# Optimization experiments

Measured on AMD Instinct MI355X. Metric: run time of the kernel, lower is better.

The kernel has to match this reference:

```python
import jax, jax.numpy as jnp
import numpy as np

ITERATIONS = 3
OUT_CAPS, OUT_DIM = 10, 16


def squash(x):
    # square_norm / (1 + square_norm) * x / (sqrt(square_norm) + 1e-6), norm over last axis
    sn = jnp.sum(x * x, axis=-1, keepdims=True)
    return sn / (1.0 + sn) * x / (jnp.sqrt(sn) + 1e-6)


def setup_inputs() -> dict:
    key = jax.random.key(0)
    kx, kw = jax.random.split(key)
    x = jax.random.normal(kx, (256, 32, 6, 6, 8), dtype=jnp.float32)
    W = 0.01 * jax.random.normal(kw, (1, 32, 6, 6, 10, 8, 16), dtype=jnp.float32)
    return {"x": x, "W": W}


def reference(x, W):
    w = W[0]  # [i,j,k,o,d,e]
    # u_hat: prediction vectors, [B, i, j, k, O, E]
    u_hat = jnp.einsum('bijkd,ijkode->bijkoe', x, w)
    u_det = jax.lax.stop_gradient(u_hat)
    b = jnp.zeros(u_hat.shape[:-1], dtype=u_hat.dtype)  # [B,i,j,k,O]
    for _ in range(ITERATIONS - 1):
        c = jax.nn.softmax(b, axis=-1)
        s = jnp.einsum('bijko,bijkoe->boe', c, u_det)   # reduce over all input-capsule axes
        v = squash(s)                                    # [B,O,E]
        b = b + jnp.einsum('bijkoe,boe->bijko', u_det, v)
    c = jax.nn.softmax(b, axis=-1)
    s = jnp.einsum('bijko,bijkoe->boe', c, u_hat)
    v = squash(s)
    return v.reshape(-1, OUT_CAPS, OUT_DIM)
```

## Files before the change

### kernel.cpp

```cpp
#include <hip/hip_runtime.h>
#include <math.h>

#define BATCH 256
#define IC    1152
#define DD    8
#define OO    10
#define EE    16
#define BTILE 128
#define NBT   2
#define NT    640
#define CHUNK 9
#define NCHUNK 128

__global__ __launch_bounds__(NT) void caps_pass_kernel(
    const float* __restrict__ x,
    const float* __restrict__ W,
    const float* __restrict__ V,
    float* __restrict__ s_part,
    int first)
{
    __shared__ float x_lds[2][DD][BTILE];
    __shared__ float logit_lds[2][2][OO][64];

    const int tid = threadIdx.x;
    const int o   = tid >> 6;
    const int bl  = tid & 63;
    const int o_u = __builtin_amdgcn_readfirstlane(o);
    const int b0  = blockIdx.y * BTILE + bl;
    const int b1  = b0 + 64;
    const int ijk0 = blockIdx.x * CHUNK;

    float v0[EE], v1[EE];
    if (first) {
        #pragma unroll
        for (int e = 0; e < EE; ++e) { v0[e] = 0.f; v1[e] = 0.f; }
    } else {
        const float4* vp0 = reinterpret_cast<const float4*>(V + ((size_t)b0 * OO + o) * EE);
        const float4* vp1 = reinterpret_cast<const float4*>(V + ((size_t)b1 * OO + o) * EE);
        #pragma unroll
        for (int q = 0; q < 4; ++q) {
            float4 t0 = vp0[q], t1 = vp1[q];
            v0[q*4+0]=t0.x; v0[q*4+1]=t0.y; v0[q*4+2]=t0.z; v0[q*4+3]=t0.w;
            v1[q*4+0]=t1.x; v1[q*4+1]=t1.y; v1[q*4+2]=t1.z; v1[q*4+3]=t1.w;
        }
    }

    float s0[EE], s1[EE];
    #pragma unroll
    for (int e = 0; e < EE; ++e) { s0[e] = 0.f; s1[e] = 0.f; }

    const bool loader = tid < BTILE * 2;
    const int lb = tid >> 1;
    const int lq = tid & 1;
    const float* xbase = x + (size_t)(blockIdx.y * BTILE + lb) * (IC * DD) + lq * 4;

    float4 xpre = make_float4(0.f, 0.f, 0.f, 0.f);
    if (loader) {
        xpre = *reinterpret_cast<const float4*>(xbase + (size_t)ijk0 * DD);
        x_lds[0][lq*4+0][lb] = xpre.x;
        x_lds[0][lq*4+1][lb] = xpre.y;
        x_lds[0][lq*4+2][lb] = xpre.z;
        x_lds[0][lq*4+3][lb] = xpre.w;
    }
    __syncthreads();

    int p = 0;
    for (int r = 0; r < CHUNK; ++r) {
        const int ijk = ijk0 + r;

        if (r + 1 < CHUNK && loader)
            xpre = *reinterpret_cast<const float4*>(xbase + (size_t)(ijk + 1) * DD);

        const float* wp = W + (size_t)ijk * (OO * DD * EE) + o_u * (DD * EE);
        float u0[EE], u1[EE];
        #pragma unroll
        for (int e = 0; e < EE; ++e) { u0[e] = 0.f; u1[e] = 0.f; }
        #pragma unroll
        for (int d = 0; d < DD; ++d) {
            float x0 = x_lds[p][d][bl];
            float x1 = x_lds[p][d][bl + 64];
            #pragma unroll
            for (int e = 0; e < EE; ++e) {
                float w = wp[d * EE + e];
                u0[e] = fmaf(x0, w, u0[e]);
                u1[e] = fmaf(x1, w, u1[e]);
            }
        }

        float lg0 = 0.f, lg1 = 0.f;
        if (!first) {
            #pragma unroll
            for (int e = 0; e < EE; ++e) {
                lg0 = fmaf(u0[e], v0[e], lg0);
                lg1 = fmaf(u1[e], v1[e], lg1);
            }
            logit_lds[p][0][o][bl] = lg0;
            logit_lds[p][1][o][bl] = lg1;
        }

        if (r + 1 < CHUNK && loader) {
            x_lds[p^1][lq*4+0][lb] = xpre.x;
            x_lds[p^1][lq*4+1][lb] = xpre.y;
            x_lds[p^1][lq*4+2][lb] = xpre.z;
            x_lds[p^1][lq*4+3][lb] = xpre.w;
        }

        __syncthreads();

        float c0, c1;
        if (first) {
            c0 = 0.1f; c1 = 0.1f;
        } else {
            float l0[OO], l1[OO];
            #pragma unroll
            for (int oo = 0; oo < OO; ++oo) {
                l0[oo] = logit_lds[p][0][oo][bl];
                l1[oo] = logit_lds[p][1][oo][bl];
            }
            float m0 = -1e30f, m1 = -1e30f;
            #pragma unroll
            for (int oo = 0; oo < OO; ++oo) {
                m0 = fmaxf(m0, l0[oo]);
                m1 = fmaxf(m1, l1[oo]);
            }
            float d0 = 0.f, d1 = 0.f;
            #pragma unroll
            for (int oo = 0; oo < OO; ++oo) {
                d0 += __expf(l0[oo] - m0);
                d1 += __expf(l1[oo] - m1);
            }
            c0 = __expf(lg0 - m0) / d0;
            c1 = __expf(lg1 - m1) / d1;
        }

        #pragma unroll
        for (int e = 0; e < EE; ++e) {
            s0[e] = fmaf(c0, u0[e], s0[e]);
            s1[e] = fmaf(c1, u1[e], s1[e]);
        }
        p ^= 1;
    }

    float* sp0 = s_part + (((size_t)blockIdx.x * BATCH + b0) * OO + o) * EE;
    float* sp1 = s_part + (((size_t)blockIdx.x * BATCH + b1) * OO + o) * EE;
    #pragma unroll
    for (int q = 0; q < 4; ++q) {
        float4 t0, t1;
        t0.x = s0[q*4+0]; t0.y = s0[q*4+1]; t0.z = s0[q*4+2]; t0.w = s0[q*4+3];
        t1.x = s1[q*4+0]; t1.y = s1[q*4+1]; t1.z = s1[q*4+2]; t1.w = s1[q*4+3];
        reinterpret_cast<float4*>(sp0)[q] = t0;
        reinterpret_cast<float4*>(sp1)[q] = t1;
    }
}

__global__ __launch_bounds__(256) void caps_squash_kernel(
    const float* __restrict__ s_part,
    float* __restrict__ V,
    float* __restrict__ out,
    int accum, int last)
{
    const int g = blockIdx.x * 256 + threadIdx.x;
    float s = 0.f;
    #pragma unroll 8
    for (int ch = 0; ch < NCHUNK; ++ch)
        s += s_part[(size_t)ch * (BATCH * OO * EE) + g];

    float sq = s * s;
    #pragma unroll
    for (int m = 1; m < 16; m <<= 1) sq += __shfl_xor(sq, m, 16);

    float scale = sq / (1.f + sq) / (sqrtf(sq) + 1e-6f);
    float v = scale * s;

    if (last)       out[g] = v;
    else if (accum) V[g]  += v;
    else            V[g]   = v;
}

extern "C" void kernel_launch(void* const* d_in, const int* in_sizes, int n_in,
                              void* d_out, int out_size, void* d_ws, size_t ws_size,
                              hipStream_t stream) {
    const float* x = (const float*)d_in[0];
    const float* W = (const float*)d_in[1];
    float* out = (float*)d_out;

    float* s_part = (float*)d_ws;
    float* V      = s_part + (size_t)NCHUNK * BATCH * OO * EE;

    dim3 grid(NCHUNK, NBT), blk(NT);
    const int sq_blocks = (BATCH * OO * EE) / 256;

    caps_pass_kernel<<<grid, blk, 0, stream>>>(x, W, V, s_part, 1);
    caps_squash_kernel<<<sq_blocks, 256, 0, stream>>>(s_part, V, out, 0, 0);
    caps_pass_kernel<<<grid, blk, 0, stream>>>(x, W, V, s_part, 0);
    caps_squash_kernel<<<sq_blocks, 256, 0, stream>>>(s_part, V, out, 1, 0);
    caps_pass_kernel<<<grid, blk, 0, stream>>>(x, W, V, s_part, 0);
    caps_squash_kernel<<<sq_blocks, 256, 0, stream>>>(s_part, V, out, 0, 1);
}
```

Baseline: 173.6 us.

## Stage full W and x chunks in LDS, drop softmax max, skip first-pass sync

Each block now loads its whole chunk of W (9 input capsules × 10×8×16 floats) and all x rows for the chunk into LDS up front, replacing the per-row global W reads and the double-buffered x prefetch. W is then read from LDS as float4, and x_lds is padded to cut bank conflicts. The softmax drops max subtraction, relying on logits staying small, and the per-row barrier now runs only on passes after the first. This adds roughly 60 KB of LDS per block, which may lower occupancy, and the unguarded exp could overflow for large logits.

```diff
diff --git a/kernel.cpp b/kernel.cpp
--- a/kernel.cpp
+++ b/kernel.cpp
@@ -11,6 +11,7 @@
 #define NT    640
 #define CHUNK 9
 #define NCHUNK 128
+#define XP    (BTILE + 1)
 
 __global__ __launch_bounds__(NT) void caps_pass_kernel(
     const float* __restrict__ x,
@@ -19,7 +20,8 @@
     float* __restrict__ s_part,
     int first)
 {
-    __shared__ float x_lds[2][DD][BTILE];
+    __shared__ __align__(16) float w_lds[CHUNK * OO * DD * EE];
+    __shared__ float x_lds[CHUNK][DD][XP];
     __shared__ float logit_lds[2][2][OO][64];
 
     const int tid = threadIdx.x;
@@ -29,6 +31,29 @@
     const int b0  = blockIdx.y * BTILE + bl;
     const int b1  = b0 + 64;
     const int ijk0 = blockIdx.x * CHUNK;
+
+    {
+        const float4* wg = reinterpret_cast<const float4*>(W + (size_t)ijk0 * (OO * DD * EE));
+        float4* wl = reinterpret_cast<float4*>(w_lds);
+        #pragma unroll
+        for (int i = 0; i < 5; ++i) {
+            int idx = tid + i * NT;
+            if (idx < (CHUNK * OO * DD * EE) / 4) wl[idx] = wg[idx];
+        }
+    }
+    for (int idx = tid; idx < CHUNK * BTILE * 2; idx += NT) {
+        int b_l = idx / (CHUNK * 2);
+        int rem = idx - b_l * (CHUNK * 2);
+        int ij  = rem >> 1;
+        int q   = rem & 1;
+        float4 t = *reinterpret_cast<const float4*>(
+            x + (size_t)(blockIdx.y * BTILE + b_l) * (IC * DD)
+              + (size_t)(ijk0 + ij) * DD + q * 4);
+        x_lds[ij][q * 4 + 0][b_l] = t.x;
+        x_lds[ij][q * 4 + 1][b_l] = t.y;
+        x_lds[ij][q * 4 + 2][b_l] = t.z;
+        x_lds[ij][q * 4 + 3][b_l] = t.w;
+    }
 
     float v0[EE], v1[EE];
     if (first) {
@@ -49,88 +74,54 @@
     #pragma unroll
     for (int e = 0; e < EE; ++e) { s0[e] = 0.f; s1[e] = 0.f; }
 
-    const bool loader = tid < BTILE * 2;
-    const int lb = tid >> 1;
-    const int lq = tid & 1;
-    const float* xbase = x + (size_t)(blockIdx.y * BTILE + lb) * (IC * DD) + lq * 4;
-
-    float4 xpre = make_float4(0.f, 0.f, 0.f, 0.f);
-    if (loader) {
-        xpre = *reinterpret_cast<const float4*>(xbase + (size_t)ijk0 * DD);
-        x_lds[0][lq*4+0][lb] = xpre.x;
-        x_lds[0][lq*4+1][lb] = xpre.y;
-        x_lds[0][lq*4+2][lb] = xpre.z;
-        x_lds[0][lq*4+3][lb] = xpre.w;
-    }
     __syncthreads();
 
-    int p = 0;
     for (int r = 0; r < CHUNK; ++r) {
-        const int ijk = ijk0 + r;
-
-        if (r + 1 < CHUNK && loader)
-            xpre = *reinterpret_cast<const float4*>(xbase + (size_t)(ijk + 1) * DD);
-
-        const float* wp = W + (size_t)ijk * (OO * DD * EE) + o_u * (DD * EE);
+        const float4* wrow = reinterpret_cast<const float4*>(
+            &w_lds[(size_t)(r * OO + o_u) * (DD * EE)]);
         float u0[EE], u1[EE];
         #pragma unroll
         for (int e = 0; e < EE; ++e) { u0[e] = 0.f; u1[e] = 0.f; }
         #pragma unroll
         for (int d = 0; d < DD; ++d) {
-            float x0 = x_lds[p][d][bl];
-            float x1 = x_lds[p][d][bl + 64];
+            float x0 = x_lds[r][d][bl];
+            float x1 = x_lds[r][d][bl + 64];
             #pragma unroll
-            for (int e = 0; e < EE; ++e) {
-                float w = wp[d * EE + e];
-                u0[e] = fmaf(x0, w, u0[e]);
-                u1[e] = fmaf(x1, w, u1[e]);
+            for (int q = 0; q < 4; ++q) {
+                float4 w4 = wrow[d * 4 + q];
+                u0[q*4+0] = fmaf(x0, w4.x, u0[q*4+0]);
+                u0[q*4+1] = fmaf(x0, w4.y, u0[q*4+1]);
+                u0[q*4+2] = fmaf(x0, w4.z, u0[q*4+2]);
+                u0[q*4+3] = fmaf(x0, w4.w, u0[q*4+3]);
+                u1[q*4+0] = fmaf(x1, w4.x, u1[q*4+0]);
+                u1[q*4+1] = fmaf(x1, w4.y, u1[q*4+1]);
+                u1[q*4+2] = fmaf(x1, w4.z, u1[q*4+2]);
+                u1[q*4+3] = fmaf(x1, w4.w, u1[q*4+3]);
             }
         }
 
-        float lg0 = 0.f, lg1 = 0.f;
-        if (!first) {
+        float c0, c1;
+        if (first) {
+            c0 = 0.1f; c1 = 0.1f;
+        } else {
+            float lg0 = 0.f, lg1 = 0.f;
             #pragma unroll
             for (int e = 0; e < EE; ++e) {
                 lg0 = fmaf(u0[e], v0[e], lg0);
                 lg1 = fmaf(u1[e], v1[e], lg1);
             }
-            logit_lds[p][0][o][bl] = lg0;
-            logit_lds[p][1][o][bl] = lg1;
-        }
-
-        if (r + 1 < CHUNK && loader) {
-            x_lds[p^1][lq*4+0][lb] = xpre.x;
-            x_lds[p^1][lq*4+1][lb] = xpre.y;
-            x_lds[p^1][lq*4+2][lb] = xpre.z;
-            x_lds[p^1][lq*4+3][lb] = xpre.w;
-        }
-
-        __syncthreads();
-
-        float c0, c1;
-        if (first) {
-            c0 = 0.1f; c1 = 0.1f;
-        } else {
-            float l0[OO], l1[OO];
-            #pragma unroll
-            for (int oo = 0; oo < OO; ++oo) {
-                l0[oo] = logit_lds[p][0][oo][bl];
-                l1[oo] = logit_lds[p][1][oo][bl];
-            }
-            float m0 = -1e30f, m1 = -1e30f;
-            #pragma unroll
-            for (int oo = 0; oo < OO; ++oo) {
-                m0 = fmaxf(m0, l0[oo]);
-                m1 = fmaxf(m1, l1[oo]);
-            }
+            const int pb = r & 1;
+            logit_lds[pb][0][o][bl] = lg0;
+            logit_lds[pb][1][o][bl] = lg1;
+            __syncthreads();
             float d0 = 0.f, d1 = 0.f;
             #pragma unroll
             for (int oo = 0; oo < OO; ++oo) {
-                d0 += __expf(l0[oo] - m0);
-                d1 += __expf(l1[oo] - m1);
+                d0 += __expf(logit_lds[pb][0][oo][bl]);
+                d1 += __expf(logit_lds[pb][1][oo][bl]);
             }
-            c0 = __expf(lg0 - m0) / d0;
-            c1 = __expf(lg1 - m1) / d1;
+            c0 = __expf(lg0) / d0;
+            c1 = __expf(lg1) / d1;
         }
 
         #pragma unroll
@@ -138,7 +129,6 @@
             s0[e] = fmaf(c0, u0[e], s0[e]);
             s1[e] = fmaf(c1, u1[e], s1[e]);
         }
-        p ^= 1;
     }
 
     float* sp0 = s_part + (((size_t)blockIdx.x * BATCH + b0) * OO + o) * EE;
```

New measurement: 174.5 us. Within noise of the previous version (+0.5%).
